# Kernel optimization log

Measured on AMD Instinct MI355X. Metric: run time of the kernel, lower is better.

## Reference

```python
import jax, jax.numpy as jnp
import numpy as np

B = 8192
D_IN = 1024
D_H = 1024


def _lin(x, w, b):
    # torch nn.Linear: y = x @ w.T + b, w: [out, in]
    return x @ w.T + b


def setup_inputs() -> dict:
    key = jax.random.key(0)
    ks = iter(jax.random.split(key, 64))
    s = 0.02

    def w(shape):
        return (jax.random.normal(next(ks), shape, dtype=jnp.float32) * s)

    inp = {
        "x": jax.random.normal(next(ks), (B, D_IN), dtype=jnp.float32),
        "h_prev": jax.random.normal(next(ks), (B, D_H), dtype=jnp.float32),
        "c_prev": jax.random.normal(next(ks), (B, D_H), dtype=jnp.float32),
    }
    for name in ["Wi", "Wf", "Wo", "Wc", "Ws"]:
        inp[name + "_w"] = w((D_H, D_IN))
        inp[name + "_b"] = w((D_H,))
    for name in ["Ui", "Uf", "Uo", "Uc", "Us"]:
        inp[name + "_w"] = w((D_H, D_H))
        inp[name + "_b"] = w((D_H,))
    # alpha_mlp: Linear(in+h -> h), ReLU, Linear(h -> 1), Sigmoid
    inp["a1_w"] = w((D_H, D_IN + D_H)); inp["a1_b"] = w((D_H,))
    inp["a2_w"] = w((1, D_H)); inp["a2_b"] = w((1,))
    inp["r1_w"] = w((D_H, D_H)); inp["r1_b"] = w((D_H,))
    inp["r2_w"] = w((D_H, D_H)); inp["r2_b"] = w((D_H,))
    inp["r3_w"] = w((D_H, D_H)); inp["r3_b"] = w((D_H,))
    return inp


def reference(x, h_prev, c_prev,
              Wi_w, Wi_b, Wf_w, Wf_b, Wo_w, Wo_b, Wc_w, Wc_b, Ws_w, Ws_b,
              Ui_w, Ui_b, Uf_w, Uf_b, Uo_w, Uo_b, Uc_w, Uc_b, Us_w, Us_b,
              a1_w, a1_b, a2_w, a2_b,
              r1_w, r1_b, r2_w, r2_b, r3_w, r3_b):
    i_t = jax.nn.sigmoid(_lin(x, Wi_w, Wi_b) + _lin(h_prev, Ui_w, Ui_b))
    f_t = jax.nn.sigmoid(_lin(x, Wf_w, Wf_b) + _lin(h_prev, Uf_w, Uf_b))
    o_t = jax.nn.sigmoid(_lin(x, Wo_w, Wo_b) + _lin(h_prev, Uo_w, Uo_b))
    c_hat_t = jnp.tanh(_lin(x, Wc_w, Wc_b) + _lin(h_prev, Uc_w, Uc_b))

    combined = jnp.concatenate([x, h_prev], axis=-1)  # [B, D_IN + D_H]
    alpha_t = jax.nn.sigmoid(_lin(jax.nn.relu(_lin(combined, a1_w, a1_b)), a2_w, a2_b))  # [B, 1]

    s_t = jax.nn.sigmoid(_lin(x, Ws_w, Ws_b) + _lin(h_prev, Us_w, Us_b))

    c_t = f_t * c_prev + i_t * c_hat_t * s_t * alpha_t

    residual = _lin(jax.nn.relu(_lin(jax.nn.relu(_lin(h_prev, r1_w, r1_b)), r2_w, r2_b)), r3_w, r3_b)
    c_t = c_t + residual
    h_t = o_t * jnp.tanh(c_t)
    return (h_t, c_t)
```

## Files before the change

### kernel.cpp

```cpp
#include <hip/hip_runtime.h>
#include <hip/hip_bf16.h>

typedef __bf16 bf16;
typedef __bf16 bf16x8 __attribute__((ext_vector_type(8)));
typedef __bf16 bf16x4 __attribute__((ext_vector_type(4)));
typedef float f32x4 __attribute__((ext_vector_type(4)));

#define NBIG 7168
#define KBIG 2048

__device__ __forceinline__ float sigmoid_f(float x) { return 1.0f / (1.0f + __expf(-x)); }
__device__ __forceinline__ float tanh_f(float x) { return 1.0f - 2.0f / (__expf(2.0f * x) + 1.0f); }

__device__ __forceinline__ void gload_lds16(const bf16* g, bf16* lds) {
  __builtin_amdgcn_global_load_lds(
      (const __attribute__((address_space(1))) unsigned int*)g,
      (__attribute__((address_space(3))) unsigned int*)lds,
      16, 0, 0);
}


__global__ __launch_bounds__(256) void build_A(const float* __restrict__ x,
                                               const float* __restrict__ h,
                                               bf16* __restrict__ A) {
  const int i4 = blockIdx.x * 256 + threadIdx.x;
  const int o = i4 * 4;
  const int m = o >> 11;
  const int c = o & 2047;
  const float4 v = (c < 1024) ? *(const float4*)&x[(size_t)m * 1024 + c]
                              : *(const float4*)&h[(size_t)m * 1024 + (c - 1024)];
  bf16x4 b;
  b[0] = (bf16)v.x; b[1] = (bf16)v.y; b[2] = (bf16)v.z; b[3] = (bf16)v.w;
  *(bf16x4*)&A[(size_t)o] = b;
}

__global__ __launch_bounds__(256) void build_WG(
    const float* __restrict__ Wi, const float* __restrict__ Wf, const float* __restrict__ Wo,
    const float* __restrict__ Wc, const float* __restrict__ Ws,
    const float* __restrict__ Ui, const float* __restrict__ Uf, const float* __restrict__ Uo,
    const float* __restrict__ Uc, const float* __restrict__ Us,
    const float* __restrict__ a1w, const float* __restrict__ r1w, bf16* __restrict__ WG) {
  const int i4 = blockIdx.x * 256 + threadIdx.x;
  const int o = i4 * 4;
  const int n = o >> 11;
  const int c = o & 2047;
  const int g = n >> 10;
  const int r = n & 1023;
  float4 v;
  if (g < 5) {
    const float* Wp = g == 0 ? Wi : g == 1 ? Wf : g == 2 ? Wo : g == 3 ? Wc : Ws;
    const float* Up = g == 0 ? Ui : g == 1 ? Uf : g == 2 ? Uo : g == 3 ? Uc : Us;
    v = (c < 1024) ? *(const float4*)&Wp[(size_t)r * 1024 + c]
                   : *(const float4*)&Up[(size_t)r * 1024 + (c - 1024)];
  } else if (g == 5) {
    v = *(const float4*)&a1w[(size_t)r * 2048 + c];
  } else {
    if (c < 1024) { v.x = 0.f; v.y = 0.f; v.z = 0.f; v.w = 0.f; }
    else v = *(const float4*)&r1w[(size_t)r * 1024 + (c - 1024)];
  }
  bf16x4 b;
  b[0] = (bf16)v.x; b[1] = (bf16)v.y; b[2] = (bf16)v.z; b[3] = (bf16)v.w;
  *(bf16x4*)&WG[(size_t)o] = b;
}

__global__ __launch_bounds__(256) void build_bias(
    const float* __restrict__ Wib, const float* __restrict__ Wfb, const float* __restrict__ Wob,
    const float* __restrict__ Wcb, const float* __restrict__ Wsb,
    const float* __restrict__ Uib, const float* __restrict__ Ufb, const float* __restrict__ Uob,
    const float* __restrict__ Ucb, const float* __restrict__ Usb,
    const float* __restrict__ a1b, const float* __restrict__ r1b, float* __restrict__ bias) {
  const int n = blockIdx.x * 256 + threadIdx.x;
  if (n >= NBIG) return;
  const int g = n >> 10, r = n & 1023;
  float v;
  if (g < 5) {
    const float* Wb = g == 0 ? Wib : g == 1 ? Wfb : g == 2 ? Wob : g == 3 ? Wcb : Wsb;
    const float* Ub = g == 0 ? Uib : g == 1 ? Ufb : g == 2 ? Uob : g == 3 ? Ucb : Usb;
    v = Wb[r] + Ub[r];
  } else if (g == 5) v = a1b[r];
  else v = r1b[r];
  bias[n] = v;
}

__global__ __launch_bounds__(256) void f2b(const float* __restrict__ s, bf16* __restrict__ d,
                                           int n4) {
  const int i = blockIdx.x * 256 + threadIdx.x;
  if (i >= n4) return;
  const float4 v = *(const float4*)&s[(size_t)i * 4];
  bf16x4 b;
  b[0] = (bf16)v.x; b[1] = (bf16)v.y; b[2] = (bf16)v.z; b[3] = (bf16)v.w;
  *(bf16x4*)&d[(size_t)i * 4] = b;
}


#define BAR __builtin_amdgcn_s_barrier()
#define VM2 asm volatile("s_waitcnt vmcnt(2)" ::: "memory")
#define VM0 asm volatile("s_waitcnt vmcnt(0)" ::: "memory")
#define PRIO1 __builtin_amdgcn_s_setprio(1)
#define PRIO0 __builtin_amdgcn_s_setprio(0)

__global__ __launch_bounds__(1024, 4) void gemm256(
    const bf16* __restrict__ A, int lda,
    const bf16* __restrict__ W, int ldw, int K,
    const float* __restrict__ bias,
    bf16* __restrict__ C, int ldc, int act_mode, int mtiles) {
  __shared__ __align__(16) bf16 sA[2][256 * 32];
  __shared__ __align__(16) bf16 sB[2][256 * 32];

  const int tid = threadIdx.x;
  const int lane = tid & 63;
  const int wv = tid >> 6;
  const int wr = wv >> 2;
  const int wc = wv & 3;

  int bmi, bni;
  if (gridDim.x == 896) {
    const int xcd = blockIdx.x & 7;
    const int idx = blockIdx.x >> 3;
    bmi = (xcd >> 2) * 16 + idx / 7;
    bni = (xcd & 3) * 7 + idx % 7;
  } else {
    bmi = blockIdx.x % mtiles;
    bni = blockIdx.x / mtiles;
  }
  const int bm = bmi * 256;
  const int bn = bni * 256;

  const int srow = tid >> 2;
  const int scol = ((tid & 3) ^ ((tid >> 3) & 3)) * 8;
  const bf16* pA = A + (size_t)(bm + srow) * lda + scol;
  const bf16* pB = W + (size_t)(bn + srow) * ldw + scol;

  const int fr = lane & 15;
  const int lg = lane >> 4;
  const int sw16 = (lg ^ ((fr >> 1) & 3)) << 4;

  const int NT = K >> 5;

  f32x4 acc[4][4] = {};
  bf16x8 ar[4], br[4];

#define STGT(bb, tt)                                                \
  do {                                                              \
    gload_lds16(pA + (size_t)(tt) * 32, &sA[bb][(wv * 16) * 32]);   \
    gload_lds16(pB + (size_t)(tt) * 32, &sB[bb][(wv * 16) * 32]);   \
  } while (0)
#define LDF(bb)                                                                  \
  do {                                                                           \
    _Pragma("unroll") for (int mi = 0; mi < 4; ++mi)                             \
        ar[mi] = *(const bf16x8*)((const char*)&sA[bb][0] +                      \
            (wr * 64 + mi * 16 + fr) * 64 + sw16);                               \
    _Pragma("unroll") for (int nj = 0; nj < 4; ++nj)                             \
        br[nj] = *(const bf16x8*)((const char*)&sB[bb][0] +                      \
            (wc * 64 + nj * 16 + fr) * 64 + sw16);                               \
  } while (0)
#define MM()                                                                     \
  do {                                                                           \
    _Pragma("unroll") for (int mi = 0; mi < 4; ++mi)                             \
    _Pragma("unroll") for (int nj = 0; nj < 4; ++nj)                             \
      acc[mi][nj] = __builtin_amdgcn_mfma_f32_16x16x32_bf16(                     \
          ar[mi], br[nj], acc[mi][nj], 0, 0, 0);                                 \
  } while (0)

  STGT(0, 0);
  STGT(1, 1);
  VM2; BAR;

  for (int t = 0; t + 2 < NT; ++t) {
    const int b = t & 1;
    LDF(b);
    PRIO1; MM(); PRIO0;
    BAR;
    STGT(b, t + 2);
    VM2;
    BAR;
  }

  {
    const int b = NT & 1;
    LDF(b);
    PRIO1; MM(); PRIO0;
    BAR; VM0; BAR;
    LDF(b ^ 1);
    PRIO1; MM(); PRIO0;
  }

  const int rbase = lg * 4;
#pragma unroll
  for (int j = 0; j < 4; ++j) {
    const int n = bn + wc * 64 + j * 16 + fr;
    const float bv = bias[n];
    const int g = (act_mode == 0) ? (n >> 10) : (act_mode == 1 ? 100 : 101);
#pragma unroll
    for (int mi = 0; mi < 4; ++mi) {
      const size_t mrow = (size_t)(bm + wr * 64 + mi * 16 + rbase);
#pragma unroll
      for (int r = 0; r < 4; ++r) {
        float v = acc[mi][j][r] + bv;
        if (g == 3) v = tanh_f(v);
        else if (g < 5) v = sigmoid_f(v);
        else if (g < 7 || g == 100) v = fmaxf(v, 0.0f);
        C[(mrow + r) * (size_t)ldc + n] = (bf16)v;
      }
    }
  }
#undef STGT
#undef LDF
#undef MM
}

__global__ __launch_bounds__(256) void gemm_bt(const bf16* __restrict__ A, int lda,
                                               const bf16* __restrict__ W, int K,
                                               const float* __restrict__ bias,
                                               bf16* __restrict__ C, int ldc, int act_mode) {
  __shared__ __align__(16) bf16 As[128 * 32];
  __shared__ __align__(16) bf16 Bs[128 * 32];

  const int tid = threadIdx.x;
  const int lane = tid & 63;
  const int wv = tid >> 6;
  const int bm = blockIdx.x * 128;
  const int bn = blockIdx.y * 128;
  const int wr = wv >> 1, wc = wv & 1;

  const int srow = wv * 16 + (lane >> 2);
  const int scol = (lane & 3) * 8;
  const bf16* ag0 = A + (size_t)(bm + srow) * lda + scol;
  const bf16* ag1 = ag0 + (size_t)64 * lda;
  const bf16* bg0 = W + (size_t)(bn + srow) * K + scol;
  const bf16* bg1 = bg0 + (size_t)64 * K;
  bf16* const al0 = &As[(wv * 16) * 32];
  bf16* const al1 = &As[(64 + wv * 16) * 32];
  bf16* const bl0 = &Bs[(wv * 16) * 32];
  bf16* const bl1 = &Bs[(64 + wv * 16) * 32];

  f32x4 acc[4][4] = {};

  const int k0 = (lane >> 4) * 8;
  const int fr = lane & 15;
  const int niter = K >> 5;
  for (int kt = 0; kt < niter; ++kt) {
    __syncthreads();
    gload_lds16(ag0, al0);
    gload_lds16(ag1, al1);
    gload_lds16(bg0, bl0);
    gload_lds16(bg1, bl1);
    ag0 += 32; ag1 += 32; bg0 += 32; bg1 += 32;
    __syncthreads();

    bf16x8 af[4], bfv[4];
#pragma unroll
    for (int f = 0; f < 4; ++f) {
      af[f] = *(const bf16x8*)&As[(wr * 64 + f * 16 + fr) * 32 + k0];
      bfv[f] = *(const bf16x8*)&Bs[(wc * 64 + f * 16 + fr) * 32 + k0];
    }
#pragma unroll
    for (int i = 0; i < 4; ++i)
#pragma unroll
      for (int j = 0; j < 4; ++j)
        acc[i][j] = __builtin_amdgcn_mfma_f32_16x16x32_bf16(af[i], bfv[j], acc[i][j], 0, 0, 0);
  }

  const int rbase = (lane >> 4) * 4;
#pragma unroll
  for (int j = 0; j < 4; ++j) {
    const int n = bn + wc * 64 + j * 16 + fr;
    const float bv = bias[n];
    const int g = (act_mode == 0) ? (n >> 10) : (act_mode == 1 ? 100 : 101);
#pragma unroll
    for (int i = 0; i < 4; ++i) {
      const size_t mrow = (size_t)(bm + wr * 64 + i * 16 + rbase);
#pragma unroll
      for (int r = 0; r < 4; ++r) {
        float v = acc[i][j][r] + bv;
        if (g == 3) v = tanh_f(v);
        else if (g < 5) v = sigmoid_f(v);
        else if (g < 7 || g == 100) v = fmaxf(v, 0.0f);
        C[(mrow + r) * (size_t)ldc + n] = (bf16)v;
      }
    }
  }
}

__global__ __launch_bounds__(256) void alpha_k(const bf16* __restrict__ G,
                                               const float* __restrict__ a2w,
                                               const float* __restrict__ a2b,
                                               float* __restrict__ alpha) {
  const int m = blockIdx.x * 4 + (threadIdx.x >> 6);
  const int lane = threadIdx.x & 63;
  const bf16* row = G + (size_t)m * NBIG + 5120 + lane * 16;
  const bf16x8 v0 = *(const bf16x8*)row;
  const bf16x8 v1 = *(const bf16x8*)(row + 8);
  const float* w = a2w + lane * 16;
  float s = 0.f;
#pragma unroll
  for (int e = 0; e < 8; ++e) s += (float)v0[e] * w[e] + (float)v1[e] * w[8 + e];
#pragma unroll
  for (int off = 32; off > 0; off >>= 1) s += __shfl_down(s, off, 64);
  if (lane == 0) alpha[m] = sigmoid_f(s + a2b[0]);
}

__global__ __launch_bounds__(256) void final_k(const bf16* __restrict__ G,
                                               const bf16* __restrict__ R3,
                                               const float* __restrict__ c_prev,
                                               const float* __restrict__ alpha,
                                               float* __restrict__ out) {
  const int idx = blockIdx.x * 256 + threadIdx.x;
  const int o = idx * 8;
  const int m = o >> 10;
  const int c = o & 1023;
  const size_t gb = (size_t)m * NBIG;
  const bf16x8 iv = *(const bf16x8*)&G[gb + c];
  const bf16x8 fv = *(const bf16x8*)&G[gb + 1024 + c];
  const bf16x8 ov = *(const bf16x8*)&G[gb + 2048 + c];
  const bf16x8 cv = *(const bf16x8*)&G[gb + 3072 + c];
  const bf16x8 sv = *(const bf16x8*)&G[gb + 4096 + c];
  const bf16x8 rv = *(const bf16x8*)&R3[(size_t)m * 1024 + c];
  const float al = alpha[m];
  const float* cp = &c_prev[(size_t)m * 1024 + c];
  float hbuf[8], cbuf[8];
#pragma unroll
  for (int e = 0; e < 8; ++e) {
    const float ct = (float)fv[e] * cp[e] + (float)iv[e] * (float)cv[e] * (float)sv[e] * al
                     + (float)rv[e];
    cbuf[e] = ct;
    hbuf[e] = (float)ov[e] * tanh_f(ct);
  }
  float* oh = out + (size_t)m * 1024 + c;
  float* oc = out + (size_t)8192 * 1024 + (size_t)m * 1024 + c;
#pragma unroll
  for (int e = 0; e < 8; ++e) { oh[e] = hbuf[e]; oc[e] = cbuf[e]; }
}

extern "C" void kernel_launch(void* const* d_in, const int* in_sizes, int n_in,
                              void* d_out, int out_size, void* d_ws, size_t ws_size,
                              hipStream_t stream) {
  const float* x      = (const float*)d_in[0];
  const float* h_prev = (const float*)d_in[1];
  const float* c_prev = (const float*)d_in[2];
  const float* Wi_w = (const float*)d_in[3];  const float* Wi_b = (const float*)d_in[4];
  const float* Wf_w = (const float*)d_in[5];  const float* Wf_b = (const float*)d_in[6];
  const float* Wo_w = (const float*)d_in[7];  const float* Wo_b = (const float*)d_in[8];
  const float* Wc_w = (const float*)d_in[9];  const float* Wc_b = (const float*)d_in[10];
  const float* Ws_w = (const float*)d_in[11]; const float* Ws_b = (const float*)d_in[12];
  const float* Ui_w = (const float*)d_in[13]; const float* Ui_b = (const float*)d_in[14];
  const float* Uf_w = (const float*)d_in[15]; const float* Uf_b = (const float*)d_in[16];
  const float* Uo_w = (const float*)d_in[17]; const float* Uo_b = (const float*)d_in[18];
  const float* Uc_w = (const float*)d_in[19]; const float* Uc_b = (const float*)d_in[20];
  const float* Us_w = (const float*)d_in[21]; const float* Us_b = (const float*)d_in[22];
  const float* a1_w = (const float*)d_in[23]; const float* a1_b = (const float*)d_in[24];
  const float* a2_w = (const float*)d_in[25]; const float* a2_b = (const float*)d_in[26];
  const float* r1_w = (const float*)d_in[27]; const float* r1_b = (const float*)d_in[28];
  const float* r2_w = (const float*)d_in[29]; const float* r2_b = (const float*)d_in[30];
  const float* r3_w = (const float*)d_in[31]; const float* r3_b = (const float*)d_in[32];

  char* ws = (char*)d_ws;
  size_t off = 0;
  auto alloc = [&](size_t bytes) -> void* {
    void* p = ws + off;
    off += (bytes + 255) & ~(size_t)255;
    return p;
  };
  bf16* A_big    = (bf16*)alloc((size_t)8192 * 2048 * 2);
  bf16* WG       = (bf16*)alloc((size_t)7168 * 2048 * 2);
  float* bias_bg = (float*)alloc((size_t)7168 * 4);
  bf16* WR2      = (bf16*)alloc((size_t)1024 * 1024 * 2);
  bf16* WR3      = (bf16*)alloc((size_t)1024 * 1024 * 2);
  bf16* G        = (bf16*)alloc((size_t)8192 * 7168 * 2);
  bf16* R2       = (bf16*)alloc((size_t)8192 * 1024 * 2);
  bf16* R3       = (bf16*)alloc((size_t)8192 * 1024 * 2);
  float* alpha   = (float*)alloc((size_t)8192 * 4);

  build_A<<<16384, 256, 0, stream>>>(x, h_prev, A_big);
  build_WG<<<14336, 256, 0, stream>>>(Wi_w, Wf_w, Wo_w, Wc_w, Ws_w,
                                      Ui_w, Uf_w, Uo_w, Uc_w, Us_w, a1_w, r1_w, WG);
  build_bias<<<28, 256, 0, stream>>>(Wi_b, Wf_b, Wo_b, Wc_b, Ws_b,
                                     Ui_b, Uf_b, Uo_b, Uc_b, Us_b, a1_b, r1_b, bias_bg);
  f2b<<<1024, 256, 0, stream>>>(r2_w, WR2, 262144);
  f2b<<<1024, 256, 0, stream>>>(r3_w, WR3, 262144);

  gemm256<<<896, 1024, 0, stream>>>(A_big, 2048, WG, 2048, 2048, bias_bg, G, NBIG, 0, 32);

  alpha_k<<<2048, 256, 0, stream>>>(G, a2_w, a2_b, alpha);

  dim3 g2(64, 8);
  gemm_bt<<<g2, 256, 0, stream>>>(G + 6144, NBIG, WR2, 1024, r2_b, R2, 1024, 1);
  gemm_bt<<<g2, 256, 0, stream>>>(R2, 1024, WR3, 1024, r3_b, R3, 1024, 2);

  final_k<<<4096, 256, 0, stream>>>(G, R3, c_prev, alpha, (float*)d_out);
}
```

Baseline: 445.3 us.

## Double GEMM K-tile depth to 64 with wider XOR swizzle

```diff
diff --git a/kernel.cpp b/kernel.cpp
--- a/kernel.cpp
+++ b/kernel.cpp
@@ -94,7 +94,7 @@
 
 
 #define BAR __builtin_amdgcn_s_barrier()
-#define VM2 asm volatile("s_waitcnt vmcnt(2)" ::: "memory")
+#define VM4 asm volatile("s_waitcnt vmcnt(4)" ::: "memory")
 #define VM0 asm volatile("s_waitcnt vmcnt(0)" ::: "memory")
 #define PRIO1 __builtin_amdgcn_s_setprio(1)
 #define PRIO0 __builtin_amdgcn_s_setprio(0)
@@ -104,8 +104,8 @@
     const bf16* __restrict__ W, int ldw, int K,
     const float* __restrict__ bias,
     bf16* __restrict__ C, int ldc, int act_mode, int mtiles) {
-  __shared__ __align__(16) bf16 sA[2][256 * 32];
-  __shared__ __align__(16) bf16 sB[2][256 * 32];
+  __shared__ __align__(16) bf16 sA[2][256 * 64];
+  __shared__ __align__(16) bf16 sB[2][256 * 64];
 
   const int tid = threadIdx.x;
   const int lane = tid & 63;
@@ -126,33 +126,37 @@
   const int bm = bmi * 256;
   const int bn = bni * 256;
 
-  const int srow = tid >> 2;
-  const int scol = ((tid & 3) ^ ((tid >> 3) & 3)) * 8;
+  const int srow = tid >> 3;
+  const int scol = ((tid & 7) ^ (srow & 7)) * 8;
   const bf16* pA = A + (size_t)(bm + srow) * lda + scol;
   const bf16* pB = W + (size_t)(bn + srow) * ldw + scol;
 
   const int fr = lane & 15;
   const int lg = lane >> 4;
-  const int sw16 = (lg ^ ((fr >> 1) & 3)) << 4;
-
-  const int NT = K >> 5;
+  const int off0 = (lg * 16) ^ ((fr & 7) << 4);
+
+  const int NT = K >> 6;
 
   f32x4 acc[4][4] = {};
   bf16x8 ar[4], br[4];
 
-#define STGT(bb, tt)                                                \
-  do {                                                              \
-    gload_lds16(pA + (size_t)(tt) * 32, &sA[bb][(wv * 16) * 32]);   \
-    gload_lds16(pB + (size_t)(tt) * 32, &sB[bb][(wv * 16) * 32]);   \
+#define STGT(bb, tt)                                                        \
+  do {                                                                      \
+    const bf16* gA = pA + (size_t)(tt) * 64;                                \
+    gload_lds16(gA, &sA[bb][(wv * 8) * 64]);                                \
+    gload_lds16(gA + (size_t)128 * lda, &sA[bb][(128 + wv * 8) * 64]);      \
+    const bf16* gB = pB + (size_t)(tt) * 64;                                \
+    gload_lds16(gB, &sB[bb][(wv * 8) * 64]);                                \
+    gload_lds16(gB + (size_t)128 * ldw, &sB[bb][(128 + wv * 8) * 64]);      \
   } while (0)
-#define LDF(bb)                                                                  \
+#define LDF(bb, kkc)                                                             \
   do {                                                                           \
     _Pragma("unroll") for (int mi = 0; mi < 4; ++mi)                             \
         ar[mi] = *(const bf16x8*)((const char*)&sA[bb][0] +                      \
-            (wr * 64 + mi * 16 + fr) * 64 + sw16);                               \
+            (wr * 64 + mi * 16 + fr) * 128 + (off0 ^ ((kkc) << 6)));             \
     _Pragma("unroll") for (int nj = 0; nj < 4; ++nj)                             \
         br[nj] = *(const bf16x8*)((const char*)&sB[bb][0] +                      \
-            (wc * 64 + nj * 16 + fr) * 64 + sw16);                               \
+            (wc * 64 + nj * 16 + fr) * 128 + (off0 ^ ((kkc) << 6)));             \
   } while (0)
 #define MM()                                                                     \
   do {                                                                           \
@@ -164,25 +168,27 @@
 
   STGT(0, 0);
   STGT(1, 1);
-  VM2; BAR;
+  VM4; BAR;
 
   for (int t = 0; t + 2 < NT; ++t) {
     const int b = t & 1;
-    LDF(b);
+    LDF(b, 0);
+    PRIO1; MM(); PRIO0;
+    LDF(b, 1);
     PRIO1; MM(); PRIO0;
     BAR;
     STGT(b, t + 2);
-    VM2;
+    VM4;
     BAR;
   }
 
   {
     const int b = NT & 1;
-    LDF(b);
-    PRIO1; MM(); PRIO0;
+    LDF(b, 0); PRIO1; MM(); PRIO0;
+    LDF(b, 1); PRIO1; MM(); PRIO0;
     BAR; VM0; BAR;
-    LDF(b ^ 1);
-    PRIO1; MM(); PRIO0;
+    LDF(b ^ 1, 0); PRIO1; MM(); PRIO0;
+    LDF(b ^ 1, 1); PRIO1; MM(); PRIO0;
   }
 
   const int rbase = lg * 4;
```

After: 410.0 us. 7.9% less time.

## Replace 256x256 GEMM with 128x128 triple-buffered kernel reused for all GEMMs

Applied to the files above, without the earlier changes.

```diff
diff --git a/kernel.cpp b/kernel.cpp
--- a/kernel.cpp
+++ b/kernel.cpp
@@ -94,37 +94,36 @@
 
 
 #define BAR __builtin_amdgcn_s_barrier()
-#define VM2 asm volatile("s_waitcnt vmcnt(2)" ::: "memory")
+#define VM4 asm volatile("s_waitcnt vmcnt(4)" ::: "memory")
 #define VM0 asm volatile("s_waitcnt vmcnt(0)" ::: "memory")
 #define PRIO1 __builtin_amdgcn_s_setprio(1)
 #define PRIO0 __builtin_amdgcn_s_setprio(0)
 
-__global__ __launch_bounds__(1024, 4) void gemm256(
+__global__ __launch_bounds__(256, 3) void gemm128(
     const bf16* __restrict__ A, int lda,
     const bf16* __restrict__ W, int ldw, int K,
     const float* __restrict__ bias,
     bf16* __restrict__ C, int ldc, int act_mode, int mtiles) {
-  __shared__ __align__(16) bf16 sA[2][256 * 32];
-  __shared__ __align__(16) bf16 sB[2][256 * 32];
+  __shared__ __align__(16) bf16 sA[3][128 * 32];
+  __shared__ __align__(16) bf16 sB[3][128 * 32];
 
   const int tid = threadIdx.x;
   const int lane = tid & 63;
   const int wv = tid >> 6;
-  const int wr = wv >> 2;
-  const int wc = wv & 3;
+  const int wr = wv >> 1, wc = wv & 1;
 
   int bmi, bni;
-  if (gridDim.x == 896) {
+  if (gridDim.x == 3584) {
     const int xcd = blockIdx.x & 7;
     const int idx = blockIdx.x >> 3;
-    bmi = (xcd >> 2) * 16 + idx / 7;
-    bni = (xcd & 3) * 7 + idx % 7;
+    bmi = (xcd >> 1) * 16 + idx / 28;
+    bni = (xcd & 1) * 28 + idx % 28;
   } else {
     bmi = blockIdx.x % mtiles;
     bni = blockIdx.x / mtiles;
   }
-  const int bm = bmi * 256;
-  const int bn = bni * 256;
+  const int bm = bmi * 128;
+  const int bn = bni * 128;
 
   const int srow = tid >> 2;
   const int scol = ((tid & 3) ^ ((tid >> 3) & 3)) * 8;
@@ -142,8 +141,14 @@
 
 #define STGT(bb, tt)                                                \
   do {                                                              \
-    gload_lds16(pA + (size_t)(tt) * 32, &sA[bb][(wv * 16) * 32]);   \
-    gload_lds16(pB + (size_t)(tt) * 32, &sB[bb][(wv * 16) * 32]);   \
+    const bf16* gA = pA + (size_t)(tt) * 32;                        \
+    bf16* lA = &sA[bb][(wv * 16) * 32];                             \
+    gload_lds16(gA, lA);                                            \
+    gload_lds16(gA + (size_t)64 * lda, lA + 64 * 32);               \
+    const bf16* gB = pB + (size_t)(tt) * 32;                        \
+    bf16* lB = &sB[bb][(wv * 16) * 32];                             \
+    gload_lds16(gB, lB);                                            \
+    gload_lds16(gB + (size_t)64 * ldw, lB + 64 * 32);               \
   } while (0)
 #define LDF(bb)                                                                  \
   do {                                                                           \
@@ -164,26 +169,26 @@
 
   STGT(0, 0);
   STGT(1, 1);
-  VM2; BAR;
-
+  VM4; BAR;
+
+  int bld = 0;
+  int bst = 2;
   for (int t = 0; t + 2 < NT; ++t) {
-    const int b = t & 1;
-    LDF(b);
+    STGT(bst, t + 2);
+    LDF(bld);
     PRIO1; MM(); PRIO0;
+    VM4;
     BAR;
-    STGT(b, t + 2);
-    VM2;
-    BAR;
-  }
-
-  {
-    const int b = NT & 1;
-    LDF(b);
-    PRIO1; MM(); PRIO0;
-    BAR; VM0; BAR;
-    LDF(b ^ 1);
-    PRIO1; MM(); PRIO0;
-  }
+    bld = bld == 2 ? 0 : bld + 1;
+    bst = bst == 2 ? 0 : bst + 1;
+  }
+
+  LDF(bld);
+  PRIO1; MM(); PRIO0;
+  VM0; BAR;
+  bld = bld == 2 ? 0 : bld + 1;
+  LDF(bld);
+  PRIO1; MM(); PRIO0;
 
   const int rbase = lg * 4;
 #pragma unroll
@@ -207,79 +212,6 @@
 #undef STGT
 #undef LDF
 #undef MM
-}
-
-__global__ __launch_bounds__(256) void gemm_bt(const bf16* __restrict__ A, int lda,
-                                               const bf16* __restrict__ W, int K,
-                                               const float* __restrict__ bias,
-                                               bf16* __restrict__ C, int ldc, int act_mode) {
-  __shared__ __align__(16) bf16 As[128 * 32];
-  __shared__ __align__(16) bf16 Bs[128 * 32];
-
-  const int tid = threadIdx.x;
-  const int lane = tid & 63;
-  const int wv = tid >> 6;
-  const int bm = blockIdx.x * 128;
-  const int bn = blockIdx.y * 128;
-  const int wr = wv >> 1, wc = wv & 1;
-
-  const int srow = wv * 16 + (lane >> 2);
-  const int scol = (lane & 3) * 8;
-  const bf16* ag0 = A + (size_t)(bm + srow) * lda + scol;
-  const bf16* ag1 = ag0 + (size_t)64 * lda;
-  const bf16* bg0 = W + (size_t)(bn + srow) * K + scol;
-  const bf16* bg1 = bg0 + (size_t)64 * K;
-  bf16* const al0 = &As[(wv * 16) * 32];
-  bf16* const al1 = &As[(64 + wv * 16) * 32];
-  bf16* const bl0 = &Bs[(wv * 16) * 32];
-  bf16* const bl1 = &Bs[(64 + wv * 16) * 32];
-
-  f32x4 acc[4][4] = {};
-
-  const int k0 = (lane >> 4) * 8;
-  const int fr = lane & 15;
-  const int niter = K >> 5;
-  for (int kt = 0; kt < niter; ++kt) {
-    __syncthreads();
-    gload_lds16(ag0, al0);
-    gload_lds16(ag1, al1);
-    gload_lds16(bg0, bl0);
-    gload_lds16(bg1, bl1);
-    ag0 += 32; ag1 += 32; bg0 += 32; bg1 += 32;
-    __syncthreads();
-
-    bf16x8 af[4], bfv[4];
-#pragma unroll
-    for (int f = 0; f < 4; ++f) {
-      af[f] = *(const bf16x8*)&As[(wr * 64 + f * 16 + fr) * 32 + k0];
-      bfv[f] = *(const bf16x8*)&Bs[(wc * 64 + f * 16 + fr) * 32 + k0];
-    }
-#pragma unroll
-    for (int i = 0; i < 4; ++i)
-#pragma unroll
-      for (int j = 0; j < 4; ++j)
-        acc[i][j] = __builtin_amdgcn_mfma_f32_16x16x32_bf16(af[i], bfv[j], acc[i][j], 0, 0, 0);
-  }
-
-  const int rbase = (lane >> 4) * 4;
-#pragma unroll
-  for (int j = 0; j < 4; ++j) {
-    const int n = bn + wc * 64 + j * 16 + fr;
-    const float bv = bias[n];
-    const int g = (act_mode == 0) ? (n >> 10) : (act_mode == 1 ? 100 : 101);
-#pragma unroll
-    for (int i = 0; i < 4; ++i) {
-      const size_t mrow = (size_t)(bm + wr * 64 + i * 16 + rbase);
-#pragma unroll
-      for (int r = 0; r < 4; ++r) {
-        float v = acc[i][j][r] + bv;
-        if (g == 3) v = tanh_f(v);
-        else if (g < 5) v = sigmoid_f(v);
-        else if (g < 7 || g == 100) v = fmaxf(v, 0.0f);
-        C[(mrow + r) * (size_t)ldc + n] = (bf16)v;
-      }
-    }
-  }
 }
 
 __global__ __launch_bounds__(256) void alpha_k(const bf16* __restrict__ G,
@@ -379,13 +311,12 @@
   f2b<<<1024, 256, 0, stream>>>(r2_w, WR2, 262144);
   f2b<<<1024, 256, 0, stream>>>(r3_w, WR3, 262144);
 
-  gemm256<<<896, 1024, 0, stream>>>(A_big, 2048, WG, 2048, 2048, bias_bg, G, NBIG, 0, 32);
+  gemm128<<<3584, 256, 0, stream>>>(A_big, 2048, WG, 2048, 2048, bias_bg, G, NBIG, 0, 64);
 
   alpha_k<<<2048, 256, 0, stream>>>(G, a2_w, a2_b, alpha);
 
-  dim3 g2(64, 8);
-  gemm_bt<<<g2, 256, 0, stream>>>(G + 6144, NBIG, WR2, 1024, r2_b, R2, 1024, 1);
-  gemm_bt<<<g2, 256, 0, stream>>>(R2, 1024, WR3, 1024, r3_b, R3, 1024, 2);
+  gemm128<<<512, 256, 0, stream>>>(G + 6144, NBIG, WR2, 1024, 1024, r2_b, R2, 1024, 1, 64);
+  gemm128<<<512, 256, 0, stream>>>(R2, 1024, WR3, 1024, 1024, r3_b, R3, 1024, 2, 64);
 
   final_k<<<4096, 256, 0, stream>>>(G, R3, c_prev, alpha, (float*)d_out);
 }
```

Measured after the change: 446.5 us. Within noise of the previous version (+0.3%).
